# Kernel tuning notes

Measured on AMD Instinct MI355X. Metric: run time of the kernel, lower is better.

## Reference

```python
import jax, jax.numpy as jnp
import numpy as np

B, C, Q, D = 64, 1024, 256, 128
NEG = -1e30  # VERY_NEGATIVE_NUMBER


def setup_inputs() -> dict:
    key = jax.random.key(0)
    k1, k2, k3, k4, k5, k6 = jax.random.split(key, 6)
    return {
        "x_cont": jax.random.normal(k1, (B, C, D), dtype=jnp.float32),
        "x_ques": jax.random.normal(k2, (B, Q, D), dtype=jnp.float32),
        "c_mask": jnp.ones((B, C), dtype=jnp.float32),
        "q_mask": jnp.ones((B, Q), dtype=jnp.float32),
        "W0": jax.random.uniform(k3, (D, 1), jnp.float32, -0.1, 0.1),
        "W1": jax.random.uniform(k4, (D, 1), jnp.float32, -0.1, 0.1),
        "W2": jax.random.uniform(k5, (1, 1, D), jnp.float32, -0.1, 0.1),
        "bias": jnp.zeros((1,), dtype=jnp.float32),
    }


def reference(x_cont, x_ques, c_mask, q_mask, W0, W1, W2, bias):
    # Trilinear similarity S[b,c,q] = x_cont.W0 + x_ques.W1 + (x_cont*W2).x_ques^T + bias
    s0 = x_cont @ W0                                   # [B,C,1]
    s1 = jnp.swapaxes(x_ques @ W1, 1, 2)               # [B,1,Q]
    s2 = jnp.einsum('bcd,bqd->bcq', x_cont * W2, x_ques)  # [B,C,Q]
    S = s0 + s1 + s2 + bias                            # [B,C,Q]

    qm = q_mask[:, None, :]                            # [B,1,Q]
    cm = c_mask[:, :, None]                            # [B,C,1]
    S_ = jax.nn.softmax(S + NEG * (1.0 - qm), axis=-1)           # row softmax [B,C,Q]
    S_T = jnp.swapaxes(jax.nn.softmax(S + NEG * (1.0 - cm), axis=1), 1, 2)  # [B,Q,C]

    c2q = S_ @ x_ques                                  # [B,C,D]
    q2c = (S_ @ S_T) @ x_cont                          # [B,C,D]
    return jnp.concatenate([x_cont, c2q, x_cont * c2q, x_cont * q2c], axis=-1)
```

## Files before the change

kernel.cpp:

```cpp
#include <hip/hip_runtime.h>
#include <math.h>

#define BB 64
#define CC 1024
#define QQ 256
#define DD 128
#define NEGV (-1.0e30f)

typedef short bf8 __attribute__((ext_vector_type(8)));
typedef short bf4 __attribute__((ext_vector_type(4)));
typedef short bf2 __attribute__((ext_vector_type(2)));
typedef float f4v __attribute__((ext_vector_type(4)));

__device__ __forceinline__ short f2bf(float f) {
    unsigned u = __builtin_bit_cast(unsigned, f);
    u += 0x7FFFu + ((u >> 16) & 1u);
    return (short)(u >> 16);
}
__device__ __forceinline__ float bf2f(short s) {
    unsigned u = ((unsigned)(unsigned short)s) << 16;
    return __builtin_bit_cast(float, u);
}

__global__ __launch_bounds__(256) void k0_pre(const float* __restrict__ xc,
                                              const float* __restrict__ xq,
                                              const float* __restrict__ W0,
                                              const float* __restrict__ W1,
                                              const float* __restrict__ W2,
                                              float* __restrict__ s0,
                                              float* __restrict__ s1,
                                              short* __restrict__ xc_bf,
                                              short* __restrict__ xqw_bf) {
    int wid = (blockIdx.x * 256 + threadIdx.x) >> 6;
    int l = threadIdx.x & 63;
    if (wid < BB * CC) {
        const float2* r = (const float2*)(xc + (size_t)wid * DD);
        float2 v = r[l];
        float2 w0 = ((const float2*)W0)[l];
        bf2 o; o.x = f2bf(v.x); o.y = f2bf(v.y);
        *(bf2*)&xc_bf[(size_t)wid * DD + 2 * l] = o;
        float acc = v.x * w0.x + v.y * w0.y;
        #pragma unroll
        for (int off = 1; off < 64; off <<= 1) acc += __shfl_xor(acc, off, 64);
        if (l == 0) s0[wid] = acc;
    } else {
        int rq = wid - BB * CC;
        const float2* r = (const float2*)(xq + (size_t)rq * DD);
        float2 v = r[l];
        float2 w1 = ((const float2*)W1)[l];
        float2 w2 = ((const float2*)W2)[l];
        bf2 o; o.x = f2bf(v.x * w2.x); o.y = f2bf(v.y * w2.y);
        *(bf2*)&xqw_bf[(size_t)rq * DD + 2 * l] = o;
        float acc = v.x * w1.x + v.y * w1.y;
        #pragma unroll
        for (int off = 1; off < 64; off <<= 1) acc += __shfl_xor(acc, off, 64);
        if (l == 0) s1[rq] = acc;
    }
}

__global__ __launch_bounds__(256) void k0_transpose(const float* __restrict__ src,
                                                    short* __restrict__ dst,
                                                    int R, int Cn) {
    __shared__ float tile[64][65];
    int tiles_r = R >> 6, tiles_c = Cn >> 6;
    int per_b = tiles_r * tiles_c;
    int b = blockIdx.x / per_b;
    int rem = blockIdx.x - b * per_b;
    int rt = rem / tiles_c;
    int ct = rem - rt * tiles_c;
    int t = threadIdx.x;
    int c4 = t & 15, rr = t >> 4;
    const float* sb = src + (size_t)b * R * Cn;
    #pragma unroll
    for (int p = 0; p < 4; ++p) {
        int ro = rr + p * 16;
        float4 g = *(const float4*)&sb[(size_t)(rt * 64 + ro) * Cn + ct * 64 + c4 * 4];
        tile[ro][c4 * 4 + 0] = g.x; tile[ro][c4 * 4 + 1] = g.y;
        tile[ro][c4 * 4 + 2] = g.z; tile[ro][c4 * 4 + 3] = g.w;
    }
    __syncthreads();
    short* db = dst + (size_t)b * R * Cn;
    #pragma unroll
    for (int p = 0; p < 4; ++p) {
        int oc = rr + p * 16;
        bf4 o;
        #pragma unroll
        for (int i = 0; i < 4; ++i) o[i] = f2bf(tile[c4 * 4 + i][oc]);
        *(bf4*)&db[(size_t)(ct * 64 + oc) * R + rt * 64 + c4 * 4] = o;
    }
}

#define SCP 1032
#define XAP 136
#define XTP 72

__global__ __launch_bounds__(256, 2) void k1_colsm(
        const short* __restrict__ xc_bf, const short* __restrict__ xcT_bf,
        const short* __restrict__ xqw_bf, const float* __restrict__ s0w,
        const float* __restrict__ c_mask, short* __restrict__ AT) {
    __shared__ __align__(16) short sc[16][SCP];
    __shared__ __align__(16) short pool[64 * XAP + 16 * XAP];
    __shared__ float s0t[64];
    __shared__ float invl[16];
    short (*xa)[XAP]  = (short(*)[XAP])pool;
    short (*xqs)[XAP] = (short(*)[XAP])(pool + 64 * XAP);
    short (*xct)[XTP] = (short(*)[XTP])pool;

    int b = blockIdx.x >> 4, qt = blockIdx.x & 15, q0 = qt * 16;
    int t = threadIdx.x, w = t >> 6, l = t & 63;
    int quad = l >> 4, l16 = l & 15;

    {
        int d8 = t & 15, q = t >> 4;
        *(bf8*)&xqs[q][d8 * 8] =
            *(const bf8*)&xqw_bf[(size_t)((b * QQ + q0 + q) * DD) + d8 * 8];
    }

    for (int ct = 0; ct < 16; ++ct) {
        __syncthreads();
        {
            int d8 = t & 15, cr = t >> 4;
            #pragma unroll
            for (int p = 0; p < 4; ++p)
                *(bf8*)&xa[cr + p * 16][d8 * 8] =
                    *(const bf8*)&xc_bf[(size_t)((b * CC + ct * 64 + cr + p * 16) * DD) + d8 * 8];
            if (t < 64)
                s0t[t] = s0w[b * CC + ct * 64 + t] + NEGV * (1.0f - c_mask[b * CC + ct * 64 + t]);
        }
        __syncthreads();
        f4v acc = {0.f, 0.f, 0.f, 0.f};
        #pragma unroll
        for (int ks = 0; ks < 4; ++ks) {
            bf8 a = *(const bf8*)&xa[w * 16 + l16][ks * 32 + quad * 8];
            bf8 bb = *(const bf8*)&xqs[l16][ks * 32 + quad * 8];
            acc = __builtin_amdgcn_mfma_f32_16x16x32_bf16(a, bb, acc, 0, 0, 0);
        }
        bf4 ov;
        #pragma unroll
        for (int r = 0; r < 4; ++r) ov[r] = f2bf(acc[r] + s0t[w * 16 + quad * 4 + r]);
        *(bf4*)&sc[l16][ct * 64 + w * 16 + quad * 4] = ov;
    }
    __syncthreads();

    {
        int q = t >> 4, k = t & 15;
        float m = -3.0e38f;
        #pragma unroll 8
        for (int i = 0; i < 64; ++i) m = fmaxf(m, bf2f(sc[q][k + 16 * i]));
        #pragma unroll
        for (int off = 1; off < 16; off <<= 1) m = fmaxf(m, __shfl_xor(m, off, 64));
        float sum = 0.f;
        #pragma unroll 8
        for (int i = 0; i < 64; ++i) {
            int idx = k + 16 * i;
            float e = __expf(bf2f(sc[q][idx]) - m);
            sc[q][idx] = f2bf(e);
            sum += e;
        }
        #pragma unroll
        for (int off = 1; off < 16; off <<= 1) sum += __shfl_xor(sum, off, 64);
        if (k == 0) invl[q] = 1.0f / sum;
    }

    f4v acc0 = {0.f, 0.f, 0.f, 0.f}, acc1 = {0.f, 0.f, 0.f, 0.f};
    for (int ct = 0; ct < 16; ++ct) {
        __syncthreads();
        {
            int c8 = t & 7, dr = t >> 3;
            #pragma unroll
            for (int p = 0; p < 4; ++p)
                *(bf8*)&xct[dr + p * 32][c8 * 8] =
                    *(const bf8*)&xcT_bf[(size_t)((b * DD + dr + p * 32) * CC) + ct * 64 + c8 * 8];
        }
        __syncthreads();
        #pragma unroll
        for (int ks = 0; ks < 2; ++ks) {
            bf8 a = *(const bf8*)&sc[l16][ct * 64 + ks * 32 + quad * 8];
            bf8 b0 = *(const bf8*)&xct[w * 32 + l16][ks * 32 + quad * 8];
            acc0 = __builtin_amdgcn_mfma_f32_16x16x32_bf16(a, b0, acc0, 0, 0, 0);
            bf8 b1 = *(const bf8*)&xct[w * 32 + 16 + l16][ks * 32 + quad * 8];
            acc1 = __builtin_amdgcn_mfma_f32_16x16x32_bf16(a, b1, acc1, 0, 0, 0);
        }
    }
    {
        bf4 o0, o1;
        #pragma unroll
        for (int r = 0; r < 4; ++r) {
            float il = invl[quad * 4 + r];
            o0[r] = f2bf(acc0[r] * il);
            o1[r] = f2bf(acc1[r] * il);
        }
        int d0 = w * 32 + l16;
        *(bf4*)&AT[(size_t)((b * DD + d0) * QQ) + q0 + quad * 4] = o0;
        *(bf4*)&AT[(size_t)((b * DD + d0 + 16) * QQ) + q0 + quad * 4] = o1;
    }
}

#define S2P 264

__global__ __launch_bounds__(256, 2) void k2_rowsm(
        const float* __restrict__ xc, const short* __restrict__ xc_bf,
        const short* __restrict__ xqw_bf, const short* __restrict__ xqT_bf,
        const short* __restrict__ AT, const float* __restrict__ s1w,
        const float* __restrict__ q_mask, float* __restrict__ out) {
    __shared__ __align__(16) short sc2[32][S2P];
    __shared__ __align__(16) short pool[32 * XAP + 64 * XAP];
    __shared__ float s1t[QQ];
    __shared__ float invl2[32];
    short (*xa2)[XAP] = (short(*)[XAP])pool;
    short (*xqt)[XAP] = (short(*)[XAP])(pool + 32 * XAP);
    short (*tT)[XTP]  = (short(*)[XTP])pool;

    int b = blockIdx.x >> 5, cb = blockIdx.x & 31, c0g = cb * 32;
    int t = threadIdx.x, w = t >> 6, l = t & 63;
    int quad = l >> 4, l16 = l & 15;

    {
        int d8 = t & 15, cr = t >> 4;
        #pragma unroll
        for (int p = 0; p < 2; ++p)
            *(bf8*)&xa2[cr + p * 16][d8 * 8] =
                *(const bf8*)&xc_bf[(size_t)((b * CC + c0g + cr + p * 16) * DD) + d8 * 8];
        s1t[t] = s1w[b * QQ + t] + NEGV * (1.0f - q_mask[b * QQ + t]);
    }

    for (int qt = 0; qt < 4; ++qt) {
        __syncthreads();
        {
            int d8 = t & 15, qr = t >> 4;
            #pragma unroll
            for (int p = 0; p < 4; ++p)
                *(bf8*)&xqt[qr + p * 16][d8 * 8] =
                    *(const bf8*)&xqw_bf[(size_t)((b * QQ + qt * 64 + qr + p * 16) * DD) + d8 * 8];
        }
        __syncthreads();
        f4v acc0 = {0.f, 0.f, 0.f, 0.f}, acc1 = {0.f, 0.f, 0.f, 0.f};
        #pragma unroll
        for (int ks = 0; ks < 4; ++ks) {
            bf8 a = *(const bf8*)&xqt[w * 16 + l16][ks * 32 + quad * 8];
            bf8 b0 = *(const bf8*)&xa2[l16][ks * 32 + quad * 8];
            acc0 = __builtin_amdgcn_mfma_f32_16x16x32_bf16(a, b0, acc0, 0, 0, 0);
            bf8 b1 = *(const bf8*)&xa2[16 + l16][ks * 32 + quad * 8];
            acc1 = __builtin_amdgcn_mfma_f32_16x16x32_bf16(a, b1, acc1, 0, 0, 0);
        }
        int qbase = qt * 64 + w * 16 + quad * 4;
        bf4 o0, o1;
        #pragma unroll
        for (int r = 0; r < 4; ++r) {
            float sv = s1t[qbase + r];
            o0[r] = f2bf(acc0[r] + sv);
            o1[r] = f2bf(acc1[r] + sv);
        }
        *(bf4*)&sc2[l16][qbase] = o0;
        *(bf4*)&sc2[16 + l16][qbase] = o1;
    }
    __syncthreads();

    {
        int c = t >> 3, k = t & 7;
        float m = -3.0e38f;
        #pragma unroll 8
        for (int i = 0; i < 32; ++i) m = fmaxf(m, bf2f(sc2[c][k + 8 * i]));
        #pragma unroll
        for (int off = 1; off < 8; off <<= 1) m = fmaxf(m, __shfl_xor(m, off, 64));
        float sum = 0.f;
        #pragma unroll 8
        for (int i = 0; i < 32; ++i) {
            int idx = k + 8 * i;
            float e = __expf(bf2f(sc2[c][idx]) - m);
            sc2[c][idx] = f2bf(e);
            sum += e;
        }
        #pragma unroll
        for (int off = 1; off < 8; off <<= 1) sum += __shfl_xor(sum, off, 64);
        if (k == 0) invl2[c] = 1.0f / sum;
    }

    int cb16 = (w & 1) * 16, dh = (w >> 1) * 64;
    f4v ac[4], aq[4];
    f4v zz = {0.f, 0.f, 0.f, 0.f};
    #pragma unroll
    for (int n = 0; n < 4; ++n) { ac[n] = zz; aq[n] = zz; }
    for (int qt = 0; qt < 4; ++qt) {
        __syncthreads();
        {
            int q8 = t & 7, dr = t >> 3;
            #pragma unroll
            for (int p = 0; p < 4; ++p)
                *(bf8*)&tT[dr + p * 32][q8 * 8] =
                    *(const bf8*)&xqT_bf[(size_t)((b * DD + dr + p * 32) * QQ) + qt * 64 + q8 * 8];
        }
        __syncthreads();
        #pragma unroll
        for (int ks = 0; ks < 2; ++ks) {
            bf8 a = *(const bf8*)&sc2[cb16 + l16][qt * 64 + ks * 32 + quad * 8];
            #pragma unroll
            for (int n = 0; n < 4; ++n) {
                bf8 bb = *(const bf8*)&tT[dh + n * 16 + l16][ks * 32 + quad * 8];
                ac[n] = __builtin_amdgcn_mfma_f32_16x16x32_bf16(a, bb, ac[n], 0, 0, 0);
            }
        }
    }
    for (int qt = 0; qt < 4; ++qt) {
        __syncthreads();
        {
            int q8 = t & 7, dr = t >> 3;
            #pragma unroll
            for (int p = 0; p < 4; ++p)
                *(bf8*)&tT[dr + p * 32][q8 * 8] =
                    *(const bf8*)&AT[(size_t)((b * DD + dr + p * 32) * QQ) + qt * 64 + q8 * 8];
        }
        __syncthreads();
        #pragma unroll
        for (int ks = 0; ks < 2; ++ks) {
            bf8 a = *(const bf8*)&sc2[cb16 + l16][qt * 64 + ks * 32 + quad * 8];
            #pragma unroll
            for (int n = 0; n < 4; ++n) {
                bf8 bb = *(const bf8*)&tT[dh + n * 16 + l16][ks * 32 + quad * 8];
                aq[n] = __builtin_amdgcn_mfma_f32_16x16x32_bf16(a, bb, aq[n], 0, 0, 0);
            }
        }
    }

    #pragma unroll
    for (int r = 0; r < 4; ++r) {
        int c = c0g + cb16 + quad * 4 + r;
        float il = invl2[cb16 + quad * 4 + r];
        const float* xrow = xc + (size_t)(b * CC + c) * DD;
        float* orow = out + (size_t)(b * CC + c) * (4 * DD);
        #pragma unroll
        for (int n = 0; n < 4; ++n) {
            int d = dh + n * 16 + l16;
            float xv = xrow[d];
            float c2v = ac[n][r] * il;
            float q2v = aq[n][r] * il;
            orow[d] = xv;
            orow[DD + d] = c2v;
            orow[2 * DD + d] = xv * c2v;
            orow[3 * DD + d] = xv * q2v;
        }
    }
}

extern "C" void kernel_launch(void* const* d_in, const int* in_sizes, int n_in,
                              void* d_out, int out_size, void* d_ws, size_t ws_size,
                              hipStream_t stream) {
    const float* x_cont = (const float*)d_in[0];
    const float* x_ques = (const float*)d_in[1];
    const float* c_mask = (const float*)d_in[2];
    const float* q_mask = (const float*)d_in[3];
    const float* W0     = (const float*)d_in[4];
    const float* W1     = (const float*)d_in[5];
    const float* W2     = (const float*)d_in[6];
    float* out = (float*)d_out;

    char* ws = (char*)d_ws;
    float* s0     = (float*)ws;  ws += (size_t)BB * CC * 4;
    float* s1     = (float*)ws;  ws += (size_t)BB * QQ * 4;
    short* xc_bf  = (short*)ws;  ws += (size_t)BB * CC * DD * 2;
    short* xqw_bf = (short*)ws;  ws += (size_t)BB * QQ * DD * 2;
    short* xcT_bf = (short*)ws;  ws += (size_t)BB * CC * DD * 2;
    short* xqT_bf = (short*)ws;  ws += (size_t)BB * QQ * DD * 2;
    short* AT     = (short*)ws;

    k0_pre<<<(BB * CC + BB * QQ) / 4, 256, 0, stream>>>(x_cont, x_ques, W0, W1, W2,
                                                        s0, s1, xc_bf, xqw_bf);
    k0_transpose<<<BB * 16 * 2, 256, 0, stream>>>(x_cont, xcT_bf, CC, DD);
    k0_transpose<<<BB * 4 * 2, 256, 0, stream>>>(x_ques, xqT_bf, QQ, DD);
    k1_colsm<<<BB * 16, 256, 0, stream>>>(xc_bf, xcT_bf, xqw_bf, s0, c_mask, AT);
    k2_rowsm<<<BB * 32, 256, 0, stream>>>(x_cont, xc_bf, xqw_bf, xqT_bf, AT, s1, q_mask, out);
}
```

Measured before the change: 299.3 us.

## Fuse preprocessing kernels and stream MFMA operands directly from global memory

Merges the bf16 conversion, dot-product and two transpose kernels into one launch that reads each input once, and folds the mask into s0/s1 there. In k1 and k2, the LDS staging loops and their barriers for the xc, xq and transposed operands are removed. MFMA operands are now loaded straight from global/L2, and the launch-bound occupancy hint goes from 2 to 4. Softmax passes use 8-wide vector LDS reads and writes. The trade is fewer syncs and LDS traffic against uncoalesced, L2-dependent global loads inside the MFMA loops.

```diff
diff --git a/kernel.cpp b/kernel.cpp
--- a/kernel.cpp
+++ b/kernel.cpp
@@ -9,7 +9,6 @@
 
 typedef short bf8 __attribute__((ext_vector_type(8)));
 typedef short bf4 __attribute__((ext_vector_type(4)));
-typedef short bf2 __attribute__((ext_vector_type(2)));
 typedef float f4v __attribute__((ext_vector_type(4)));
 
 __device__ __forceinline__ short f2bf(float f) {
@@ -22,89 +21,91 @@
     return __builtin_bit_cast(float, u);
 }
 
-__global__ __launch_bounds__(256) void k0_pre(const float* __restrict__ xc,
-                                              const float* __restrict__ xq,
-                                              const float* __restrict__ W0,
-                                              const float* __restrict__ W1,
-                                              const float* __restrict__ W2,
-                                              float* __restrict__ s0,
-                                              float* __restrict__ s1,
-                                              short* __restrict__ xc_bf,
-                                              short* __restrict__ xqw_bf) {
-    int wid = (blockIdx.x * 256 + threadIdx.x) >> 6;
-    int l = threadIdx.x & 63;
-    if (wid < BB * CC) {
-        const float2* r = (const float2*)(xc + (size_t)wid * DD);
-        float2 v = r[l];
-        float2 w0 = ((const float2*)W0)[l];
-        bf2 o; o.x = f2bf(v.x); o.y = f2bf(v.y);
-        *(bf2*)&xc_bf[(size_t)wid * DD + 2 * l] = o;
-        float acc = v.x * w0.x + v.y * w0.y;
-        #pragma unroll
-        for (int off = 1; off < 64; off <<= 1) acc += __shfl_xor(acc, off, 64);
-        if (l == 0) s0[wid] = acc;
+__global__ __launch_bounds__(256) void k0_fused(
+        const float* __restrict__ xc, const float* __restrict__ xq,
+        const float* __restrict__ W0, const float* __restrict__ W1,
+        const float* __restrict__ W2,
+        const float* __restrict__ c_mask, const float* __restrict__ q_mask,
+        float* __restrict__ s0m, float* __restrict__ s1m,
+        short* __restrict__ xc_bf, short* __restrict__ xqw_bf,
+        short* __restrict__ xcT_bf, short* __restrict__ xqT_bf) {
+    __shared__ float tile[64][132];
+    int t = threadIdx.x;
+    int r = t >> 2, seg = t & 3;
+    int d = t >> 1, half = t & 1;
+
+    if (blockIdx.x < BB * (CC / 64)) {
+        int b = blockIdx.x >> 4, rt = blockIdx.x & 15;
+        int row = b * CC + rt * 64 + r;
+        const float4* src = (const float4*)(xc + (size_t)row * DD + seg * 32);
+        const float4* w0 = (const float4*)(W0 + seg * 32);
+        short* dst = xc_bf + (size_t)row * DD + seg * 32;
+        float acc = 0.f;
+        #pragma unroll
+        for (int i = 0; i < 8; i++) {
+            float4 v = src[i];
+            float4 w = w0[i];
+            acc += v.x * w.x + v.y * w.y + v.z * w.z + v.w * w.w;
+            bf4 o; o[0] = f2bf(v.x); o[1] = f2bf(v.y); o[2] = f2bf(v.z); o[3] = f2bf(v.w);
+            *(bf4*)&dst[i * 4] = o;
+            *(float4*)&tile[r][seg * 32 + i * 4] = v;
+        }
+        acc += __shfl_xor(acc, 1, 64);
+        acc += __shfl_xor(acc, 2, 64);
+        if (seg == 0) s0m[row] = acc + NEGV * (1.0f - c_mask[row]);
+        __syncthreads();
+        short* drow = xcT_bf + ((size_t)(b * DD + d)) * CC + rt * 64 + half * 32;
+        #pragma unroll
+        for (int jj = 0; jj < 4; jj++) {
+            bf8 o;
+            #pragma unroll
+            for (int i = 0; i < 8; i++) o[i] = f2bf(tile[half * 32 + jj * 8 + i][d]);
+            *(bf8*)&drow[jj * 8] = o;
+        }
     } else {
-        int rq = wid - BB * CC;
-        const float2* r = (const float2*)(xq + (size_t)rq * DD);
-        float2 v = r[l];
-        float2 w1 = ((const float2*)W1)[l];
-        float2 w2 = ((const float2*)W2)[l];
-        bf2 o; o.x = f2bf(v.x * w2.x); o.y = f2bf(v.y * w2.y);
-        *(bf2*)&xqw_bf[(size_t)rq * DD + 2 * l] = o;
-        float acc = v.x * w1.x + v.y * w1.y;
-        #pragma unroll
-        for (int off = 1; off < 64; off <<= 1) acc += __shfl_xor(acc, off, 64);
-        if (l == 0) s1[rq] = acc;
-    }
-}
-
-__global__ __launch_bounds__(256) void k0_transpose(const float* __restrict__ src,
-                                                    short* __restrict__ dst,
-                                                    int R, int Cn) {
-    __shared__ float tile[64][65];
-    int tiles_r = R >> 6, tiles_c = Cn >> 6;
-    int per_b = tiles_r * tiles_c;
-    int b = blockIdx.x / per_b;
-    int rem = blockIdx.x - b * per_b;
-    int rt = rem / tiles_c;
-    int ct = rem - rt * tiles_c;
-    int t = threadIdx.x;
-    int c4 = t & 15, rr = t >> 4;
-    const float* sb = src + (size_t)b * R * Cn;
-    #pragma unroll
-    for (int p = 0; p < 4; ++p) {
-        int ro = rr + p * 16;
-        float4 g = *(const float4*)&sb[(size_t)(rt * 64 + ro) * Cn + ct * 64 + c4 * 4];
-        tile[ro][c4 * 4 + 0] = g.x; tile[ro][c4 * 4 + 1] = g.y;
-        tile[ro][c4 * 4 + 2] = g.z; tile[ro][c4 * 4 + 3] = g.w;
-    }
-    __syncthreads();
-    short* db = dst + (size_t)b * R * Cn;
-    #pragma unroll
-    for (int p = 0; p < 4; ++p) {
-        int oc = rr + p * 16;
-        bf4 o;
-        #pragma unroll
-        for (int i = 0; i < 4; ++i) o[i] = f2bf(tile[c4 * 4 + i][oc]);
-        *(bf4*)&db[(size_t)(ct * 64 + oc) * R + rt * 64 + c4 * 4] = o;
+        int id = blockIdx.x - BB * (CC / 64);
+        int b = id >> 2, rt = id & 3;
+        int row = b * QQ + rt * 64 + r;
+        const float4* src = (const float4*)(xq + (size_t)row * DD + seg * 32);
+        const float4* w1 = (const float4*)(W1 + seg * 32);
+        const float4* w2 = (const float4*)(W2 + seg * 32);
+        short* dst = xqw_bf + (size_t)row * DD + seg * 32;
+        float acc = 0.f;
+        #pragma unroll
+        for (int i = 0; i < 8; i++) {
+            float4 v = src[i];
+            float4 w = w1[i];
+            float4 m = w2[i];
+            acc += v.x * w.x + v.y * w.y + v.z * w.z + v.w * w.w;
+            bf4 o; o[0] = f2bf(v.x * m.x); o[1] = f2bf(v.y * m.y);
+                   o[2] = f2bf(v.z * m.z); o[3] = f2bf(v.w * m.w);
+            *(bf4*)&dst[i * 4] = o;
+            *(float4*)&tile[r][seg * 32 + i * 4] = v;
+        }
+        acc += __shfl_xor(acc, 1, 64);
+        acc += __shfl_xor(acc, 2, 64);
+        if (seg == 0) s1m[row] = acc + NEGV * (1.0f - q_mask[row]);
+        __syncthreads();
+        short* drow = xqT_bf + ((size_t)(b * DD + d)) * QQ + rt * 64 + half * 32;
+        #pragma unroll
+        for (int jj = 0; jj < 4; jj++) {
+            bf8 o;
+            #pragma unroll
+            for (int i = 0; i < 8; i++) o[i] = f2bf(tile[half * 32 + jj * 8 + i][d]);
+            *(bf8*)&drow[jj * 8] = o;
+        }
     }
 }
 
 #define SCP 1032
-#define XAP 136
-#define XTP 72
-
-__global__ __launch_bounds__(256, 2) void k1_colsm(
+
+__global__ __launch_bounds__(256, 4) void k1_colsm(
         const short* __restrict__ xc_bf, const short* __restrict__ xcT_bf,
-        const short* __restrict__ xqw_bf, const float* __restrict__ s0w,
-        const float* __restrict__ c_mask, short* __restrict__ AT) {
+        const short* __restrict__ xqw_bf, const float* __restrict__ s0m,
+        short* __restrict__ AT) {
     __shared__ __align__(16) short sc[16][SCP];
-    __shared__ __align__(16) short pool[64 * XAP + 16 * XAP];
-    __shared__ float s0t[64];
+    __shared__ __align__(16) short xqs[16][136];
     __shared__ float invl[16];
-    short (*xa)[XAP]  = (short(*)[XAP])pool;
-    short (*xqs)[XAP] = (short(*)[XAP])(pool + 64 * XAP);
-    short (*xct)[XTP] = (short(*)[XTP])pool;
 
     int b = blockIdx.x >> 4, qt = blockIdx.x & 15, q0 = qt * 16;
     int t = threadIdx.x, w = t >> 6, l = t & 63;
@@ -113,31 +114,23 @@
     {
         int d8 = t & 15, q = t >> 4;
         *(bf8*)&xqs[q][d8 * 8] =
-            *(const bf8*)&xqw_bf[(size_t)((b * QQ + q0 + q) * DD) + d8 * 8];
-    }
-
+            *(const bf8*)&xqw_bf[((size_t)(b * QQ + q0 + q)) * DD + d8 * 8];
+    }
+    __syncthreads();
+
+    const short* aBase = xc_bf + ((size_t)(b * CC + w * 16 + l16)) * DD + quad * 8;
     for (int ct = 0; ct < 16; ++ct) {
-        __syncthreads();
-        {
-            int d8 = t & 15, cr = t >> 4;
-            #pragma unroll
-            for (int p = 0; p < 4; ++p)
-                *(bf8*)&xa[cr + p * 16][d8 * 8] =
-                    *(const bf8*)&xc_bf[(size_t)((b * CC + ct * 64 + cr + p * 16) * DD) + d8 * 8];
-            if (t < 64)
-                s0t[t] = s0w[b * CC + ct * 64 + t] + NEGV * (1.0f - c_mask[b * CC + ct * 64 + t]);
-        }
-        __syncthreads();
         f4v acc = {0.f, 0.f, 0.f, 0.f};
         #pragma unroll
         for (int ks = 0; ks < 4; ++ks) {
-            bf8 a = *(const bf8*)&xa[w * 16 + l16][ks * 32 + quad * 8];
+            bf8 a = *(const bf8*)(aBase + (size_t)ct * 64 * DD + ks * 32);
             bf8 bb = *(const bf8*)&xqs[l16][ks * 32 + quad * 8];
             acc = __builtin_amdgcn_mfma_f32_16x16x32_bf16(a, bb, acc, 0, 0, 0);
         }
+        float4 sv = *(const float4*)&s0m[b * CC + ct * 64 + w * 16 + quad * 4];
         bf4 ov;
-        #pragma unroll
-        for (int r = 0; r < 4; ++r) ov[r] = f2bf(acc[r] + s0t[w * 16 + quad * 4 + r]);
+        ov[0] = f2bf(acc[0] + sv.x); ov[1] = f2bf(acc[1] + sv.y);
+        ov[2] = f2bf(acc[2] + sv.z); ov[3] = f2bf(acc[3] + sv.w);
         *(bf4*)&sc[l16][ct * 64 + w * 16 + quad * 4] = ov;
     }
     __syncthreads();
@@ -145,42 +138,42 @@
     {
         int q = t >> 4, k = t & 15;
         float m = -3.0e38f;
-        #pragma unroll 8
-        for (int i = 0; i < 64; ++i) m = fmaxf(m, bf2f(sc[q][k + 16 * i]));
+        #pragma unroll
+        for (int p = 0; p < 8; ++p) {
+            bf8 v8 = *(const bf8*)&sc[q][p * 128 + k * 8];
+            #pragma unroll
+            for (int i = 0; i < 8; ++i) m = fmaxf(m, bf2f(v8[i]));
+        }
         #pragma unroll
         for (int off = 1; off < 16; off <<= 1) m = fmaxf(m, __shfl_xor(m, off, 64));
         float sum = 0.f;
-        #pragma unroll 8
-        for (int i = 0; i < 64; ++i) {
-            int idx = k + 16 * i;
-            float e = __expf(bf2f(sc[q][idx]) - m);
-            sc[q][idx] = f2bf(e);
-            sum += e;
+        #pragma unroll
+        for (int p = 0; p < 8; ++p) {
+            bf8 v8 = *(const bf8*)&sc[q][p * 128 + k * 8];
+            bf8 e8;
+            #pragma unroll
+            for (int i = 0; i < 8; ++i) {
+                float e = __expf(bf2f(v8[i]) - m);
+                e8[i] = f2bf(e);
+                sum += e;
+            }
+            *(bf8*)&sc[q][p * 128 + k * 8] = e8;
         }
         #pragma unroll
         for (int off = 1; off < 16; off <<= 1) sum += __shfl_xor(sum, off, 64);
         if (k == 0) invl[q] = 1.0f / sum;
     }
-
+    __syncthreads();
+
+    const short* bBase0 = xcT_bf + ((size_t)(b * DD + w * 32 + l16)) * CC + quad * 8;
+    const short* bBase1 = bBase0 + (size_t)16 * CC;
     f4v acc0 = {0.f, 0.f, 0.f, 0.f}, acc1 = {0.f, 0.f, 0.f, 0.f};
-    for (int ct = 0; ct < 16; ++ct) {
-        __syncthreads();
-        {
-            int c8 = t & 7, dr = t >> 3;
-            #pragma unroll
-            for (int p = 0; p < 4; ++p)
-                *(bf8*)&xct[dr + p * 32][c8 * 8] =
-                    *(const bf8*)&xcT_bf[(size_t)((b * DD + dr + p * 32) * CC) + ct * 64 + c8 * 8];
-        }
-        __syncthreads();
-        #pragma unroll
-        for (int ks = 0; ks < 2; ++ks) {
-            bf8 a = *(const bf8*)&sc[l16][ct * 64 + ks * 32 + quad * 8];
-            bf8 b0 = *(const bf8*)&xct[w * 32 + l16][ks * 32 + quad * 8];
-            acc0 = __builtin_amdgcn_mfma_f32_16x16x32_bf16(a, b0, acc0, 0, 0, 0);
-            bf8 b1 = *(const bf8*)&xct[w * 32 + 16 + l16][ks * 32 + quad * 8];
-            acc1 = __builtin_amdgcn_mfma_f32_16x16x32_bf16(a, b1, acc1, 0, 0, 0);
-        }
+    for (int ks = 0; ks < 32; ++ks) {
+        bf8 a = *(const bf8*)&sc[l16][ks * 32 + quad * 8];
+        bf8 b0 = *(const bf8*)(bBase0 + ks * 32);
+        acc0 = __builtin_amdgcn_mfma_f32_16x16x32_bf16(a, b0, acc0, 0, 0, 0);
+        bf8 b1 = *(const bf8*)(bBase1 + ks * 32);
+        acc1 = __builtin_amdgcn_mfma_f32_16x16x32_bf16(a, b1, acc1, 0, 0, 0);
     }
     {
         bf4 o0, o1;
@@ -191,25 +184,21 @@
             o1[r] = f2bf(acc1[r] * il);
         }
         int d0 = w * 32 + l16;
-        *(bf4*)&AT[(size_t)((b * DD + d0) * QQ) + q0 + quad * 4] = o0;
-        *(bf4*)&AT[(size_t)((b * DD + d0 + 16) * QQ) + q0 + quad * 4] = o1;
+        *(bf4*)&AT[((size_t)(b * DD + d0)) * QQ + q0 + quad * 4] = o0;
+        *(bf4*)&AT[((size_t)(b * DD + d0 + 16)) * QQ + q0 + quad * 4] = o1;
     }
 }
 
 #define S2P 264
 
-__global__ __launch_bounds__(256, 2) void k2_rowsm(
+__global__ __launch_bounds__(256, 4) void k2_rowsm(
         const float* __restrict__ xc, const short* __restrict__ xc_bf,
         const short* __restrict__ xqw_bf, const short* __restrict__ xqT_bf,
-        const short* __restrict__ AT, const float* __restrict__ s1w,
-        const float* __restrict__ q_mask, float* __restrict__ out) {
+        const short* __restrict__ AT, const float* __restrict__ s1m,
+        float* __restrict__ out) {
     __shared__ __align__(16) short sc2[32][S2P];
-    __shared__ __align__(16) short pool[32 * XAP + 64 * XAP];
-    __shared__ float s1t[QQ];
+    __shared__ __align__(16) short xa2[32][136];
     __shared__ float invl2[32];
-    short (*xa2)[XAP] = (short(*)[XAP])pool;
-    short (*xqt)[XAP] = (short(*)[XAP])(pool + 32 * XAP);
-    short (*tT)[XTP]  = (short(*)[XTP])pool;
 
     int b = blockIdx.x >> 5, cb = blockIdx.x & 31, c0g = cb * 32;
     int t = threadIdx.x, w = t >> 6, l = t & 63;
@@ -220,37 +209,28 @@
         #pragma unroll
         for (int p = 0; p < 2; ++p)
             *(bf8*)&xa2[cr + p * 16][d8 * 8] =
-                *(const bf8*)&xc_bf[(size_t)((b * CC + c0g + cr + p * 16) * DD) + d8 * 8];
-        s1t[t] = s1w[b * QQ + t] + NEGV * (1.0f - q_mask[b * QQ + t]);
-    }
-
+                *(const bf8*)&xc_bf[((size_t)(b * CC + c0g + cr + p * 16)) * DD + d8 * 8];
+    }
+    __syncthreads();
+
+    const short* aQ = xqw_bf + ((size_t)(b * QQ + w * 16 + l16)) * DD + quad * 8;
     for (int qt = 0; qt < 4; ++qt) {
-        __syncthreads();
-        {
-            int d8 = t & 15, qr = t >> 4;
-            #pragma unroll
-            for (int p = 0; p < 4; ++p)
-                *(bf8*)&xqt[qr + p * 16][d8 * 8] =
-                    *(const bf8*)&xqw_bf[(size_t)((b * QQ + qt * 64 + qr + p * 16) * DD) + d8 * 8];
-        }
-        __syncthreads();
-        f4v acc0 = {0.f, 0.f, 0.f, 0.f}, acc1 = {0.f, 0.f, 0.f, 0.f};
+        f4v a0 = {0.f, 0.f, 0.f, 0.f}, a1 = {0.f, 0.f, 0.f, 0.f};
         #pragma unroll
         for (int ks = 0; ks < 4; ++ks) {
-            bf8 a = *(const bf8*)&xqt[w * 16 + l16][ks * 32 + quad * 8];
+            bf8 a = *(const bf8*)(aQ + (size_t)qt * 64 * DD + ks * 32);
             bf8 b0 = *(const bf8*)&xa2[l16][ks * 32 + quad * 8];
-            acc0 = __builtin_amdgcn_mfma_f32_16x16x32_bf16(a, b0, acc0, 0, 0, 0);
+            a0 = __builtin_amdgcn_mfma_f32_16x16x32_bf16(a, b0, a0, 0, 0, 0);
             bf8 b1 = *(const bf8*)&xa2[16 + l16][ks * 32 + quad * 8];
-            acc1 = __builtin_amdgcn_mfma_f32_16x16x32_bf16(a, b1, acc1, 0, 0, 0);
+            a1 = __builtin_amdgcn_mfma_f32_16x16x32_bf16(a, b1, a1, 0, 0, 0);
         }
         int qbase = qt * 64 + w * 16 + quad * 4;
+        float4 sv = *(const float4*)&s1m[b * QQ + qbase];
         bf4 o0, o1;
-        #pragma unroll
-        for (int r = 0; r < 4; ++r) {
-            float sv = s1t[qbase + r];
-            o0[r] = f2bf(acc0[r] + sv);
-            o1[r] = f2bf(acc1[r] + sv);
-        }
+        o0[0] = f2bf(a0[0] + sv.x); o0[1] = f2bf(a0[1] + sv.y);
+        o0[2] = f2bf(a0[2] + sv.z); o0[3] = f2bf(a0[3] + sv.w);
+        o1[0] = f2bf(a1[0] + sv.x); o1[1] = f2bf(a1[1] + sv.y);
+        o1[2] = f2bf(a1[2] + sv.z); o1[3] = f2bf(a1[3] + sv.w);
         *(bf4*)&sc2[l16][qbase] = o0;
         *(bf4*)&sc2[16 + l16][qbase] = o1;
     }
@@ -259,66 +239,51 @@
     {
         int c = t >> 3, k = t & 7;
         float m = -3.0e38f;
-        #pragma unroll 8
-        for (int i = 0; i < 32; ++i) m = fmaxf(m, bf2f(sc2[c][k + 8 * i]));
+        #pragma unroll
+        for (int p = 0; p < 4; ++p) {
+            bf8 v8 = *(const bf8*)&sc2[c][p * 64 + k * 8];
+            #pragma unroll
+            for (int i = 0; i < 8; ++i) m = fmaxf(m, bf2f(v8[i]));
+        }
         #pragma unroll
         for (int off = 1; off < 8; off <<= 1) m = fmaxf(m, __shfl_xor(m, off, 64));
         float sum = 0.f;
-        #pragma unroll 8
-        for (int i = 0; i < 32; ++i) {
-            int idx = k + 8 * i;
-            float e = __expf(bf2f(sc2[c][idx]) - m);
-            sc2[c][idx] = f2bf(e);
-            sum += e;
+        #pragma unroll
+        for (int p = 0; p < 4; ++p) {
+            bf8 v8 = *(const bf8*)&sc2[c][p * 64 + k * 8];
+            bf8 e8;
+            #pragma unroll
+            for (int i = 0; i < 8; ++i) {
+                float e = __expf(bf2f(v8[i]) - m);
+                e8[i] = f2bf(e);
+                sum += e;
+            }
+            *(bf8*)&sc2[c][p * 64 + k * 8] = e8;
         }
         #pragma unroll
         for (int off = 1; off < 8; off <<= 1) sum += __shfl_xor(sum, off, 64);
         if (k == 0) invl2[c] = 1.0f / sum;
     }
+    __syncthreads();
 
     int cb16 = (w & 1) * 16, dh = (w >> 1) * 64;
+    const short* bQ = xqT_bf + ((size_t)(b * DD + dh + l16)) * QQ + quad * 8;
+    const short* bA = AT + ((size_t)(b * DD + dh + l16)) * QQ + quad * 8;
     f4v ac[4], aq[4];
     f4v zz = {0.f, 0.f, 0.f, 0.f};
     #pragma unroll
     for (int n = 0; n < 4; ++n) { ac[n] = zz; aq[n] = zz; }
-    for (int qt = 0; qt < 4; ++qt) {
-        __syncthreads();
-        {
-            int q8 = t & 7, dr = t >> 3;
-            #pragma unroll
-            for (int p = 0; p < 4; ++p)
-                *(bf8*)&tT[dr + p * 32][q8 * 8] =
-                    *(const bf8*)&xqT_bf[(size_t)((b * DD + dr + p * 32) * QQ) + qt * 64 + q8 * 8];
-        }
-        __syncthreads();
-        #pragma unroll
-        for (int ks = 0; ks < 2; ++ks) {
-            bf8 a = *(const bf8*)&sc2[cb16 + l16][qt * 64 + ks * 32 + quad * 8];
-            #pragma unroll
-            for (int n = 0; n < 4; ++n) {
-                bf8 bb = *(const bf8*)&tT[dh + n * 16 + l16][ks * 32 + quad * 8];
-                ac[n] = __builtin_amdgcn_mfma_f32_16x16x32_bf16(a, bb, ac[n], 0, 0, 0);
-            }
-        }
-    }
-    for (int qt = 0; qt < 4; ++qt) {
-        __syncthreads();
-        {
-            int q8 = t & 7, dr = t >> 3;
-            #pragma unroll
-            for (int p = 0; p < 4; ++p)
-                *(bf8*)&tT[dr + p * 32][q8 * 8] =
-                    *(const bf8*)&AT[(size_t)((b * DD + dr + p * 32) * QQ) + qt * 64 + q8 * 8];
-        }
-        __syncthreads();
-        #pragma unroll
-        for (int ks = 0; ks < 2; ++ks) {
-            bf8 a = *(const bf8*)&sc2[cb16 + l16][qt * 64 + ks * 32 + quad * 8];
-            #pragma unroll
-            for (int n = 0; n < 4; ++n) {
-                bf8 bb = *(const bf8*)&tT[dh + n * 16 + l16][ks * 32 + quad * 8];
-                aq[n] = __builtin_amdgcn_mfma_f32_16x16x32_bf16(a, bb, aq[n], 0, 0, 0);
-            }
+    for (int qs = 0; qs < 8; ++qs) {
+        bf8 a = *(const bf8*)&sc2[cb16 + l16][qs * 32 + quad * 8];
+        #pragma unroll
+        for (int n = 0; n < 4; ++n) {
+            bf8 bb = *(const bf8*)(bQ + (size_t)n * 16 * QQ + qs * 32);
+            ac[n] = __builtin_amdgcn_mfma_f32_16x16x32_bf16(a, bb, ac[n], 0, 0, 0);
+        }
+        #pragma unroll
+        for (int n = 0; n < 4; ++n) {
+            bf8 bb = *(const bf8*)(bA + (size_t)n * 16 * QQ + qs * 32);
+            aq[n] = __builtin_amdgcn_mfma_f32_16x16x32_bf16(a, bb, aq[n], 0, 0, 0);
         }
     }
 
@@ -355,18 +320,17 @@
     float* out = (float*)d_out;
 
     char* ws = (char*)d_ws;
-    float* s0     = (float*)ws;  ws += (size_t)BB * CC * 4;
-    float* s1     = (float*)ws;  ws += (size_t)BB * QQ * 4;
+    float* s0m    = (float*)ws;  ws += (size_t)BB * CC * 4;
+    float* s1m    = (float*)ws;  ws += (size_t)BB * QQ * 4;
     short* xc_bf  = (short*)ws;  ws += (size_t)BB * CC * DD * 2;
     short* xqw_bf = (short*)ws;  ws += (size_t)BB * QQ * DD * 2;
     short* xcT_bf = (short*)ws;  ws += (size_t)BB * CC * DD * 2;
     short* xqT_bf = (short*)ws;  ws += (size_t)BB * QQ * DD * 2;
     short* AT     = (short*)ws;
 
-    k0_pre<<<(BB * CC + BB * QQ) / 4, 256, 0, stream>>>(x_cont, x_ques, W0, W1, W2,
-                                                        s0, s1, xc_bf, xqw_bf);
-    k0_transpose<<<BB * 16 * 2, 256, 0, stream>>>(x_cont, xcT_bf, CC, DD);
-    k0_transpose<<<BB * 4 * 2, 256, 0, stream>>>(x_ques, xqT_bf, QQ, DD);
-    k1_colsm<<<BB * 16, 256, 0, stream>>>(xc_bf, xcT_bf, xqw_bf, s0, c_mask, AT);
-    k2_rowsm<<<BB * 32, 256, 0, stream>>>(x_cont, xc_bf, xqw_bf, xqT_bf, AT, s1, q_mask, out);
-}
+    k0_fused<<<BB * (CC / 64) + BB * (QQ / 64), 256, 0, stream>>>(
+        x_cont, x_ques, W0, W1, W2, c_mask, q_mask,
+        s0m, s1m, xc_bf, xqw_bf, xcT_bf, xqT_bf);
+    k1_colsm<<<BB * 16, 256, 0, stream>>>(xc_bf, xcT_bf, xqw_bf, s0m, AT);
+    k2_rowsm<<<BB * 32, 256, 0, stream>>>(x_cont, xc_bf, xqw_bf, xqT_bf, AT, s1m, out);
+}
```

Result: slower. 317.5 us (+6.1%).
